# Kernel tuning notes

Hardware: AMD Instinct MI355X
Metric: run time of the kernel (lower is better)

Reference implementation:

```python
import jax, jax.numpy as jnp
import numpy as np
from jax import lax

WS = 8
NH = 16

def _conv1x1(t, w):
    # w: (Cout, Cin), t: (B,C,H,W)
    return jnp.einsum('oc,bchw->bohw', w, t)

def _bn(t, g, b, m, v, eps=1e-5):
    s = g * lax.rsqrt(v + eps)
    return (t - m[:, None, None]) * s[:, None, None] + b[:, None, None]

def _forward(x, qkv_w, l2_w, bn2_g, bn2_b, bn2_m, bn2_v, wq, wk, wv, rel_x, rel_y,
             l1_bias, rel_table, dw_w, bnp_g, bnp_b, bnp_m, bnp_v, pw_w):
    B, C, H, W = x.shape
    ws, nh = WS, NH
    d = C // nh
    scale = d ** -0.5

    # ---- local2: 1x1 conv + BN (inference) ----
    local = _bn(_conv1x1(x, l2_w), bn2_g, bn2_b, bn2_m, bn2_v)

    # ---- local1: SelfAttentionConv2d, k=3, pad=1, groups=1 ----
    xp = jnp.pad(x, ((0, 0), (0, 0), (1, 1), (1, 1)))  # zero pad
    vq = _conv1x1(xp, wq)
    vk = _conv1x1(xp, wk)
    vv = _conv1x1(xp, wv)
    win_q = vq[:, :, 1:H + 1, 1:W + 1]  # center crop -> (B,C,H,W)
    def patches3(t):
        p = jnp.stack([t[:, :, i:i + H, j:j + W] for i in range(3) for j in range(3)], axis=-1)
        return p.reshape(B, C, H, W, 3, 3)
    pk = patches3(vk)
    pv = patches3(vv)
    rs = C // 2
    qx = jnp.einsum('bxhw,xk->bhwk', win_q[:, :rs], rel_x)  # (B,H,W,3)
    qy = jnp.einsum('byhw,yk->bhwk', win_q[:, rs:], rel_y)
    logits = jnp.einsum('bchw,bchwkl->bhwkl', win_q, pk)
    logits = logits + qx[:, :, :, None, :] + qy[:, :, :, :, None]
    a = jax.nn.softmax(logits.reshape(B, H, W, 9), axis=-1).reshape(B, H, W, 3, 3)
    local = local + jnp.einsum('bhwkl,bchwkl->bchw', a, pv) + l1_bias[None, :, None, None]

    # ---- windowed MHSA (H, W divisible by ws so pad() is a no-op) ----
    qkv = _conv1x1(x, qkv_w)  # (B, 3C, H, W)
    hh, ww = H // ws, W // ws
    t = qkv.reshape(B, 3, nh, d, hh, ws, ww, ws)
    t = t.transpose(1, 0, 4, 6, 2, 5, 7, 3).reshape(3, B * hh * ww, nh, ws * ws, d)
    q, k, v = t[0], t[1], t[2]
    dots = jnp.einsum('wnid,wnjd->wnij', q, k) * scale
    # relative position bias
    coords = np.stack(np.meshgrid(np.arange(ws), np.arange(ws), indexing='ij')).reshape(2, -1)
    rel = (coords[:, :, None] - coords[:, None, :]).transpose(1, 2, 0) + (ws - 1)
    idx = rel[..., 0] * (2 * ws - 1) + rel[..., 1]  # (ws*ws, ws*ws)
    rpb = rel_table[idx.reshape(-1)].reshape(ws * ws, ws * ws, nh).transpose(2, 0, 1)
    dots = dots + rpb[None]
    attn = jnp.einsum('wnij,wnjd->wnid', jax.nn.softmax(dots, axis=-1), v)
    attn = attn.reshape(B, hh, ww, nh, ws, ws, d).transpose(0, 3, 6, 1, 4, 2, 5).reshape(B, C, H, W)

    # ---- pooling edge-correction branches ----
    pad_h = jnp.pad(attn, ((0, 0), (0, 0), (0, 1), (0, 0)), mode='reflect')
    pad_w = jnp.pad(attn, ((0, 0), (0, 0), (0, 0), (0, 1)), mode='reflect')
    p = ws // 2 - 1
    mph = lax.reduce_window(pad_h, -jnp.inf, lax.max, (1, 1, ws, 1), (1, 1, 1, 1),
                            [(0, 0), (0, 0), (p, p), (0, 0)])
    mpw = lax.reduce_window(pad_w, -jnp.inf, lax.max, (1, 1, 1, ws), (1, 1, 1, 1),
                            [(0, 0), (0, 0), (0, 0), (p, p)])
    aph = lax.reduce_window(pad_h, 0.0, lax.add, (1, 1, ws, 1), (1, 1, 1, 1),
                            [(0, 0), (0, 0), (p, p), (0, 0)]) / ws
    apw = lax.reduce_window(pad_w, 0.0, lax.add, (1, 1, 1, ws), (1, 1, 1, 1),
                            [(0, 0), (0, 0), (0, 0), (p, p)]) / ws
    out = mph + mpw + aph + apw + local

    # ---- proj: reflect pad_out + depthwise 8x8 conv (pad 3) + BN + 1x1 ----
    out = jnp.pad(out, ((0, 0), (0, 0), (0, 1), (0, 1)), mode='reflect')
    out = lax.conv_general_dilated(out, dw_w, (1, 1), [(3, 3), (3, 3)],
                                   dimension_numbers=('NCHW', 'OIHW', 'NCHW'),
                                   feature_group_count=C)
    out = _bn(out, bnp_g, bnp_b, bnp_m, bnp_v)
    out = _conv1x1(out, pw_w)
    return out[:, :, :H, :W]


def setup_inputs() -> dict:
    key = jax.random.key(0)
    ks = jax.random.split(key, 20)
    C = 256
    n = lambda k, shp, s=1.0: jax.random.normal(k, shp, dtype=jnp.float32) * s
    u = lambda k, shp: jax.random.uniform(k, shp, dtype=jnp.float32, minval=0.5, maxval=1.5)
    fan = 1.0 / 16.0  # 1/sqrt(256)
    return {
        'x': n(ks[0], (2, C, 96, 96)),
        'qkv_w': n(ks[1], (3 * C, C), fan),
        'l2_w': n(ks[2], (C, C), fan),
        'bn2_g': u(ks[3], (C,)), 'bn2_b': n(ks[4], (C,), 0.1),
        'bn2_m': n(ks[5], (C,), 0.1), 'bn2_v': u(ks[6], (C,)),
        'wq': n(ks[7], (C, C), fan), 'wk': n(ks[8], (C, C), fan), 'wv': n(ks[9], (C, C), fan),
        'rel_x': n(ks[10], (C // 2, 3), 0.1), 'rel_y': n(ks[11], (C // 2, 3), 0.1),
        'l1_bias': n(ks[12], (C,), 0.05),
        'rel_table': n(ks[13], (15 * 15, NH), 0.02),
        'dw_w': n(ks[14], (C, 1, 8, 8), 1.0 / 8.0),
        'bnp_g': u(ks[15], (C,)), 'bnp_b': n(ks[16], (C,), 0.1),
        'bnp_m': n(ks[17], (C,), 0.1), 'bnp_v': u(ks[18], (C,)),
        'pw_w': n(ks[19], (C, C), fan),
    }


def reference(x, qkv_w, l2_w, bn2_g, bn2_b, bn2_m, bn2_v, wq, wk, wv, rel_x, rel_y,
              l1_bias, rel_table, dw_w, bnp_g, bnp_b, bnp_m, bnp_v, pw_w):
    return _forward(x, qkv_w, l2_w, bn2_g, bn2_b, bn2_m, bn2_v, wq, wk, wv, rel_x, rel_y,
                    l1_bias, rel_table, dw_w, bnp_g, bnp_b, bnp_m, bnp_v, pw_w)
```

## Files before the change

kernel.cpp:

```cpp
#include <hip/hip_runtime.h>
#include <math.h>


namespace {

constexpr int NP = 96 * 96;
constexpr int C  = 256;

typedef __bf16 bf16x8 __attribute__((ext_vector_type(8)));
typedef __bf16 bf16x4 __attribute__((ext_vector_type(4)));
typedef float  f32x4  __attribute__((ext_vector_type(4)));
typedef float  f32x16 __attribute__((ext_vector_type(16)));

__device__ __forceinline__ unsigned short f2bf_rne(float f) {
  unsigned u = __float_as_uint(f);
  u += 0x7FFFu + ((u >> 16) & 1u);
  return (unsigned short)(u >> 16);
}
__device__ __forceinline__ __bf16 f2bf16(float f) {
  unsigned short s = f2bf_rne(f);
  return *(__bf16*)&s;
}
__device__ __forceinline__ float bf2f(unsigned short s) {
  unsigned u = (unsigned)s << 16;
  return __uint_as_float(u);
}
__device__ __forceinline__ float4 bf4_to_f4(const unsigned short* p) {
  bf16x4 v = *(const bf16x4*)p;
  float4 r;
  r.x = (float)v[0]; r.y = (float)v[1]; r.z = (float)v[2]; r.w = (float)v[3];
  return r;
}

__global__ __launch_bounds__(256) void prep(
    const float* __restrict__ x,
    const float* __restrict__ l2, const float* __restrict__ q,
    const float* __restrict__ k,  const float* __restrict__ v,
    const float* __restrict__ qkv, const float* __restrict__ pw,
    unsigned short* __restrict__ XT, unsigned short* __restrict__ W7)
{
  __shared__ float tile[64][65];
  const int bx = blockIdx.x;
  const int t = threadIdx.x;
  if (bx < 2048) {
    const int row = bx;
    const float* src; int r;
    if      (row <  256) { src = l2;  r = row; }
    else if (row <  512) { src = q;   r = row - 256; }
    else if (row <  768) { src = k;   r = row - 512; }
    else if (row < 1024) { src = v;   r = row - 768; }
    else if (row < 1792) { src = qkv; r = row - 1024; }
    else                 { src = pw;  r = row - 1792; }
    W7[row * 256 + t] = f2bf_rne(src[r * 256 + t]);
    return;
  }
  const int xb = bx - 2048;
  const int p0 = (xb % 144) * 64;
  const int c0 = ((xb / 144) % 4) * 64;
  const int b  = xb / 576;
  const float* xb_p = x + (long)b * C * NP;
#pragma unroll
  for (int i = 0; i < 4; ++i) {
    int s = i * 256 + t;
    int c = s >> 4, p4 = s & 15;
    float4 vv = *(const float4*)&xb_p[(long)(c0 + c) * NP + p0 + p4 * 4];
    tile[c][p4 * 4 + 0] = vv.x;
    tile[c][p4 * 4 + 1] = vv.y;
    tile[c][p4 * 4 + 2] = vv.z;
    tile[c][p4 * 4 + 3] = vv.w;
  }
  __syncthreads();
  unsigned short* XTb = XT + (long)b * NP * 256;
#pragma unroll
  for (int i = 0; i < 2; ++i) {
    int s = i * 256 + t;
    int p = s >> 3, c8 = s & 7;
    unsigned short u[8];
#pragma unroll
    for (int e = 0; e < 8; ++e) u[e] = f2bf_rne(tile[c8 * 8 + e][p]);
    *(uint4*)&XTb[(long)(p0 + p) * 256 + c0 + c8 * 8] = *(const uint4*)u;
  }
}

__global__ __launch_bounds__(256) void xpose(
    const float* __restrict__ x, unsigned short* __restrict__ XT)
{
  __shared__ float tile[64][65];
  const int t = threadIdx.x;
  const int p0 = blockIdx.x * 64, c0 = blockIdx.y * 64, b = blockIdx.z;
  const float* xb = x + (long)b * C * NP;
#pragma unroll
  for (int i = 0; i < 4; ++i) {
    int s = i * 256 + t;
    int c = s >> 4, p4 = s & 15;
    float4 v = *(const float4*)&xb[(long)(c0 + c) * NP + p0 + p4 * 4];
    tile[c][p4 * 4 + 0] = v.x;
    tile[c][p4 * 4 + 1] = v.y;
    tile[c][p4 * 4 + 2] = v.z;
    tile[c][p4 * 4 + 3] = v.w;
  }
  __syncthreads();
  unsigned short* XTb = XT + (long)b * NP * 256;
#pragma unroll
  for (int i = 0; i < 2; ++i) {
    int s = i * 256 + t;
    int p = s >> 3, c8 = s & 7;
    unsigned short u[8];
#pragma unroll
    for (int e = 0; e < 8; ++e) u[e] = f2bf_rne(tile[c8 * 8 + e][p]);
    *(uint4*)&XTb[(long)(p0 + p) * 256 + c0 + c8 * 8] = *(const uint4*)u;
  }
}

__device__ __forceinline__ void gemm_bt_body(
    unsigned short* smemS,
    const unsigned short* __restrict__ W, const unsigned short* __restrict__ XTb,
    unsigned short* __restrict__ Ob, int Mstride, int m0, int n0)
{
  unsigned short* As = smemS;
  unsigned short* Bs = smemS + 4096;

  const int t = threadIdx.x;
  const int lane = t & 63, wid = t >> 6;
  const int wm = wid >> 1, wn = wid & 1;
  const int l15 = lane & 15, l4 = lane >> 4;
  const int crow = lane >> 2;
  const int ccol = (lane & 3) * 8;

  f32x4 acc[4][4];
#pragma unroll
  for (int i = 0; i < 4; ++i)
#pragma unroll
    for (int j = 0; j < 4; ++j) acc[i][j] = (f32x4){0.f, 0.f, 0.f, 0.f};

  for (int k0 = 0; k0 < 256; k0 += 32) {
#pragma unroll
    for (int i = 0; i < 4; ++i) {
      const int ch = wid * 4 + i;
      if (ch < 8) {
        const int row = ch * 16 + crow;
        __builtin_amdgcn_global_load_lds(
            (const __attribute__((address_space(1))) unsigned int*)
                &W[(long)(m0 + row) * 256 + k0 + ccol],
            (__attribute__((address_space(3))) unsigned int*)&As[ch * 512],
            16, 0, 0);
      } else {
        const int row = (ch - 8) * 16 + crow;
        __builtin_amdgcn_global_load_lds(
            (const __attribute__((address_space(1))) unsigned int*)
                &XTb[(long)(n0 + row) * 256 + k0 + ccol],
            (__attribute__((address_space(3))) unsigned int*)&Bs[(ch - 8) * 512],
            16, 0, 0);
      }
    }
    __syncthreads();

    bf16x8 af[4], bb[4];
#pragma unroll
    for (int mf = 0; mf < 4; ++mf)
      af[mf] = *(const bf16x8*)&As[(wm * 64 + mf * 16 + l15) * 32 + l4 * 8];
#pragma unroll
    for (int nf = 0; nf < 4; ++nf)
      bb[nf] = *(const bf16x8*)&Bs[(wn * 64 + nf * 16 + l15) * 32 + l4 * 8];
#pragma unroll
    for (int mf = 0; mf < 4; ++mf)
#pragma unroll
      for (int nf = 0; nf < 4; ++nf)
        acc[mf][nf] = __builtin_amdgcn_mfma_f32_16x16x32_bf16(
            af[mf], bb[nf], acc[mf][nf], 0, 0, 0);
    __syncthreads();
  }

  unsigned short* trw = smemS + wid * 64 * 72;
#pragma unroll
  for (int mf = 0; mf < 4; ++mf)
#pragma unroll
    for (int nf = 0; nf < 4; ++nf) {
      unsigned u0 = (unsigned)f2bf_rne(acc[mf][nf][0]) |
                    ((unsigned)f2bf_rne(acc[mf][nf][1]) << 16);
      unsigned u1 = (unsigned)f2bf_rne(acc[mf][nf][2]) |
                    ((unsigned)f2bf_rne(acc[mf][nf][3]) << 16);
      uint2 uu; uu.x = u0; uu.y = u1;
      *(uint2*)&trw[(nf * 16 + l15) * 72 + mf * 16 + l4 * 4] = uu;
    }
  __syncthreads();

  const long pix = n0 + wn * 64 + lane;
  const long rowbase = pix * Mstride + m0 + wm * 64;
#pragma unroll
  for (int cc = 0; cc < 8; ++cc)
    *(uint4*)&Ob[rowbase + cc * 8] = *(const uint4*)&trw[lane * 72 + cc * 8];
}

__global__ __launch_bounds__(256) void gemm_bt(
    const unsigned short* __restrict__ W, const unsigned short* __restrict__ XT,
    unsigned short* __restrict__ O, int Mstride)
{
  __shared__ __align__(16) unsigned short smemS[18432];
  gemm_bt_body(smemS, W, XT + (long)blockIdx.z * NP * 256,
               O + (long)blockIdx.z * NP * Mstride, Mstride,
               blockIdx.y * 128, blockIdx.x * 128);
}

__device__ __forceinline__ void local_attn_body(
    char* smem,
    const unsigned short* __restrict__ GA, int b, int tile,
    const float* __restrict__ rel_x, const float* __restrict__ rel_y,
    const float* __restrict__ bn2_g, const float* __restrict__ bn2_b,
    const float* __restrict__ bn2_m, const float* __restrict__ bn2_v,
    const float* __restrict__ l1_bias, unsigned short* __restrict__ localO)
{
  float (*red)[32][13] = reinterpret_cast<float(*)[32][13]>(smem);
  float* srel  = (float*)(smem + 13312);
  float* sS    = (float*)(smem + 16384);
  float* sO    = sS + 256;
  float* sBias = sO + 256;

  const int t = threadIdx.x;
  const int px = t & 31, ch = t >> 5;
  const int ty = tile / 24, tx = tile % 24;
  const int h = ty * 8 + (px >> 2), w = tx * 4 + (px & 3);
  const int p = h * 96 + w;
  const unsigned short* Gb = GA + (long)b * NP * 1024;

  if (t < 128) {
    srel[t * 3 + 0] = rel_x[t * 3 + 0];
    srel[t * 3 + 1] = rel_x[t * 3 + 1];
    srel[t * 3 + 2] = rel_x[t * 3 + 2];
  } else {
    int r = t - 128;
    srel[t * 3 + 0] = rel_y[r * 3 + 0];
    srel[t * 3 + 1] = rel_y[r * 3 + 1];
    srel[t * 3 + 2] = rel_y[r * 3 + 2];
  }
  {
    float s = bn2_g[t] * rsqrtf(bn2_v[t] + 1e-5f);
    sS[t] = s;
    sO[t] = bn2_b[t] - bn2_m[t] * s;
    sBias[t] = l1_bias[t];
  }

  int nof[9];
  float msk[9];
#pragma unroll
  for (int ky = 0; ky < 3; ++ky)
#pragma unroll
    for (int kx = 0; kx < 3; ++kx) {
      int j = ky * 3 + kx, hn = h + ky - 1, wn = w + kx - 1;
      bool v = (hn >= 0 && hn < 96 && wn >= 0 && wn < 96);
      nof[j] = v ? hn * 96 + wn : p;
      msk[j] = v ? 1.f : 0.f;
    }
  __syncthreads();

  float lg[9] = {0, 0, 0, 0, 0, 0, 0, 0, 0};
  float rq[3] = {0, 0, 0};
  const int c0 = ch * 32;
#pragma unroll
  for (int i = 0; i < 4; ++i) {
    const int c = c0 + i * 8;
    bf16x8 q8 = *(const bf16x8*)&Gb[(long)p * 1024 + 256 + c];
    float qv[8];
#pragma unroll
    for (int e = 0; e < 8; ++e) qv[e] = (float)q8[e];
#pragma unroll
    for (int j = 0; j < 9; ++j) {
      bf16x8 k8 = *(const bf16x8*)&Gb[(long)nof[j] * 1024 + 512 + c];
#pragma unroll
      for (int e = 0; e < 8; ++e) lg[j] += qv[e] * (float)k8[e];
    }
#pragma unroll
    for (int e = 0; e < 8; ++e) {
      const float* sr = &srel[(c + e) * 3];
      rq[0] += qv[e] * sr[0];
      rq[1] += qv[e] * sr[1];
      rq[2] += qv[e] * sr[2];
    }
  }
#pragma unroll
  for (int j = 0; j < 9; ++j) red[ch][px][j] = lg[j] * msk[j];
#pragma unroll
  for (int l = 0; l < 3; ++l) red[ch][px][9 + l] = rq[l];
  __syncthreads();

  float a[9];
  float mx = -1e30f;
#pragma unroll
  for (int j = 0; j < 9; ++j) {
    float v = 0.f;
#pragma unroll
    for (int u = 0; u < 8; ++u) v += red[u][px][j];
    float qxl = red[0][px][9 + j % 3] + red[1][px][9 + j % 3] +
                red[2][px][9 + j % 3] + red[3][px][9 + j % 3];
    float qyk = red[4][px][9 + j / 3] + red[5][px][9 + j / 3] +
                red[6][px][9 + j / 3] + red[7][px][9 + j / 3];
    a[j] = v + qxl + qyk;
    mx = fmaxf(mx, a[j]);
  }
  float sum = 0.f;
#pragma unroll
  for (int j = 0; j < 9; ++j) { a[j] = __expf(a[j] - mx); sum += a[j]; }
  const float inv = 1.f / sum;
  float am[9];
#pragma unroll
  for (int j = 0; j < 9; ++j) am[j] = a[j] * inv * msk[j];

#pragma unroll
  for (int i = 0; i < 4; ++i) {
    const int c = c0 + i * 8;
    bf16x8 l28 = *(const bf16x8*)&Gb[(long)p * 1024 + 0 + c];
    float o8[8] = {0, 0, 0, 0, 0, 0, 0, 0};
#pragma unroll
    for (int j = 0; j < 9; ++j) {
      bf16x8 v8 = *(const bf16x8*)&Gb[(long)nof[j] * 1024 + 768 + c];
#pragma unroll
      for (int e = 0; e < 8; ++e) o8[e] += am[j] * (float)v8[e];
    }
#pragma unroll
    for (int e = 0; e < 8; ++e) {
      const int cg = c + e;
      localO[((long)b * C + cg) * NP + p] = f2bf_rne(
          (float)l28[e] * sS[cg] + sO[cg] + o8[e] + sBias[cg]);
    }
  }
}

__global__ __launch_bounds__(256) void la_qkv(
    const unsigned short* __restrict__ Wqkv, const unsigned short* __restrict__ XT,
    unsigned short* __restrict__ GB, const unsigned short* __restrict__ GA,
    const float* __restrict__ rel_x, const float* __restrict__ rel_y,
    const float* __restrict__ bn2_g, const float* __restrict__ bn2_b,
    const float* __restrict__ bn2_m, const float* __restrict__ bn2_v,
    const float* __restrict__ l1_bias, unsigned short* __restrict__ localO)
{
  __shared__ __align__(16) char smem[36864];
  const int bx = blockIdx.x;
  if (bx < 864) {
    const int n = bx % 72, rest = bx / 72;
    const int m = rest % 6, b = rest / 6;
    gemm_bt_body((unsigned short*)smem, Wqkv, XT + (long)b * NP * 256,
                 GB + (long)b * NP * 768, 768, m * 128, n * 128);
  } else {
    const int idx = bx - 864;
    const int orig = idx % 288, b = idx / 288;
    const int tile = (orig & 7) * 36 + (orig >> 3);
    local_attn_body(smem, GA, b, tile, rel_x, rel_y, bn2_g, bn2_b, bn2_m,
                    bn2_v, l1_bias, localO);
  }
}

__global__ __launch_bounds__(256) void gemm_cf32(
    const unsigned short* __restrict__ W, const unsigned short* __restrict__ XT,
    float* __restrict__ Co)
{
  __shared__ unsigned short As[64][40];
  __shared__ unsigned short Bs[128][40];

  const int t = threadIdx.x;
  const int lane = t & 63, wid = t >> 6;
  const int wm = wid >> 1, wn = wid & 1;
  const int l15 = lane & 15, l4 = lane >> 4;
  const int n0 = blockIdx.x * 128, m0 = blockIdx.y * 64;
  const unsigned short* XTb = XT + (long)blockIdx.z * NP * 256;
  float* Cb = Co + (long)blockIdx.z * C * NP;

  f32x4 acc[2][4];
#pragma unroll
  for (int i = 0; i < 2; ++i)
#pragma unroll
    for (int j = 0; j < 4; ++j) acc[i][j] = (f32x4){0.f, 0.f, 0.f, 0.f};

  for (int k0 = 0; k0 < 256; k0 += 32) {
    {
      int r = t >> 2, kc = t & 3;
      *(uint4*)&As[r][kc * 8] =
          *(const uint4*)&W[(long)(m0 + r) * 256 + k0 + kc * 8];
    }
#pragma unroll
    for (int i = 0; i < 2; ++i) {
      int s = i * 256 + t, r = s >> 2, kc = s & 3;
      *(uint4*)&Bs[r][kc * 8] =
          *(const uint4*)&XTb[(long)(n0 + r) * 256 + k0 + kc * 8];
    }
    __syncthreads();

    bf16x8 af[2], bb[4];
#pragma unroll
    for (int mf = 0; mf < 2; ++mf)
      af[mf] = *(const bf16x8*)&As[wm * 32 + mf * 16 + l15][l4 * 8];
#pragma unroll
    for (int nf = 0; nf < 4; ++nf)
      bb[nf] = *(const bf16x8*)&Bs[wn * 64 + nf * 16 + l15][l4 * 8];
#pragma unroll
    for (int mf = 0; mf < 2; ++mf)
#pragma unroll
      for (int nf = 0; nf < 4; ++nf)
        acc[mf][nf] = __builtin_amdgcn_mfma_f32_16x16x32_bf16(
            af[mf], bb[nf], acc[mf][nf], 0, 0, 0);
    __syncthreads();
  }

#pragma unroll
  for (int mf = 0; mf < 2; ++mf)
#pragma unroll
    for (int r = 0; r < 4; ++r) {
      int row = m0 + wm * 32 + mf * 16 + l4 * 4 + r;
#pragma unroll
      for (int nf = 0; nf < 4; ++nf) {
        int col = n0 + wn * 64 + nf * 16 + l15;
        Cb[(long)row * NP + col] = acc[mf][nf][r];
      }
    }
}

__global__ __launch_bounds__(64) void window_attn_mfma(
    const unsigned short* __restrict__ QKV,
    const float* __restrict__ rel_table, unsigned short* __restrict__ attnO)
{
  const int win = blockIdx.x, hd = blockIdx.y, b = blockIdx.z;
  const int wy = win / 12, wx = win % 12;
  const int lane = threadIdx.x;
  const int l15 = lane & 15, hi4 = lane >> 4;
  const int l31 = lane & 31, hi2 = lane >> 5;

  __shared__ float srpb[225];
  __shared__ __bf16 P[64][72];

  for (int i = lane; i < 225; i += 64) srpb[i] = rel_table[i * 16 + hd];

  const __bf16* base = (const __bf16*)QKV + (long)b * 9216 * 768;
  const int pixbase = (wy * 8) * 96 + wx * 8;

#define WPIX(i) (pixbase + ((i) >> 3) * 96 + ((i) & 7))

  bf16x8 kf[2], qf[2];
#pragma unroll
  for (int kt = 0; kt < 2; ++kt)
    kf[kt] = *(const bf16x8*)&base[(long)WPIX(32 * kt + l31) * 768 + 256 +
                                   hd * 16 + hi2 * 8];
#pragma unroll
  for (int qt = 0; qt < 2; ++qt)
    qf[qt] = *(const bf16x8*)&base[(long)WPIX(32 * qt + l31) * 768 +
                                   hd * 16 + hi2 * 8];

  bf16x8 vf[2];
#pragma unroll
  for (int kc = 0; kc < 2; ++kc)
#pragma unroll
    for (int j = 0; j < 8; ++j)
      vf[kc][j] = base[(long)WPIX(32 * kc + 8 * hi4 + j) * 768 + 512 +
                       hd * 16 + l15];

  f32x16 S[2][2];
#pragma unroll
  for (int kt = 0; kt < 2; ++kt)
#pragma unroll
    for (int qt = 0; qt < 2; ++qt)
#pragma unroll
      for (int r = 0; r < 16; ++r) S[kt][qt][r] = 0.f;

#pragma unroll
  for (int kt = 0; kt < 2; ++kt)
#pragma unroll
    for (int qt = 0; qt < 2; ++qt)
      S[kt][qt] = __builtin_amdgcn_mfma_f32_32x32x16_bf16(
          kf[kt], qf[qt], S[kt][qt], 0, 0, 0);

  __syncthreads();

  float mx[2] = {-1e30f, -1e30f};
#pragma unroll
  for (int kt = 0; kt < 2; ++kt)
#pragma unroll
    for (int r = 0; r < 16; ++r) {
      const int key = 32 * kt + (r & 3) + 8 * (r >> 2) + 4 * hi2;
      const int ky = key >> 3, kx = key & 7;
#pragma unroll
      for (int qt = 0; qt < 2; ++qt) {
        const int q = 32 * qt + l31;
        const int qy = q >> 3, qx = q & 7;
        float s = S[kt][qt][r] * 0.25f + srpb[(qy - ky + 7) * 15 + (qx - kx + 7)];
        S[kt][qt][r] = s;
        mx[qt] = fmaxf(mx[qt], s);
      }
    }
#pragma unroll
  for (int qt = 0; qt < 2; ++qt)
    mx[qt] = fmaxf(mx[qt], __shfl_xor(mx[qt], 32));

  float sum[2] = {0.f, 0.f};
#pragma unroll
  for (int kt = 0; kt < 2; ++kt)
#pragma unroll
    for (int qt = 0; qt < 2; ++qt)
#pragma unroll
      for (int r = 0; r < 16; ++r) {
        float e = __expf(S[kt][qt][r] - mx[qt]);
        S[kt][qt][r] = e;
        sum[qt] += e;
      }
#pragma unroll
  for (int qt = 0; qt < 2; ++qt) sum[qt] += __shfl_xor(sum[qt], 32);
  const float inv0 = 1.f / sum[0], inv1 = 1.f / sum[1];

#pragma unroll
  for (int qt = 0; qt < 2; ++qt) {
    const float inv = qt ? inv1 : inv0;
#pragma unroll
    for (int kt = 0; kt < 2; ++kt)
#pragma unroll
      for (int rq = 0; rq < 4; ++rq) {
        bf16x4 pk;
#pragma unroll
        for (int j = 0; j < 4; ++j) pk[j] = f2bf16(S[kt][qt][rq * 4 + j] * inv);
        *(bf16x4*)&P[32 * qt + l31][32 * kt + 8 * rq + 4 * hi2] = pk;
      }
  }
  __syncthreads();

  f32x4 o[4];
#pragma unroll
  for (int qt4 = 0; qt4 < 4; ++qt4) o[qt4] = (f32x4){0.f, 0.f, 0.f, 0.f};
#pragma unroll
  for (int kc = 0; kc < 2; ++kc)
#pragma unroll
    for (int qt4 = 0; qt4 < 4; ++qt4) {
      bf16x8 pf = *(const bf16x8*)&P[16 * qt4 + l15][32 * kc + 8 * hi4];
      o[qt4] = __builtin_amdgcn_mfma_f32_16x16x32_bf16(vf[kc], pf, o[qt4], 0, 0, 0);
    }

#pragma unroll
  for (int qt4 = 0; qt4 < 4; ++qt4)
#pragma unroll
    for (int r = 0; r < 4; ++r) {
      const int q = 16 * qt4 + l15;
      attnO[((long)b * C + hd * 16 + 4 * hi4 + r) * NP + WPIX(q)] =
          f2bf_rne(o[qt4][r]);
    }
#undef WPIX
}

__global__ __launch_bounds__(128) void pool_dw8(
    const unsigned short* __restrict__ attn,
    const unsigned short* __restrict__ localO,
    const float* __restrict__ dww,
    const float* __restrict__ bnp_g, const float* __restrict__ bnp_b,
    const float* __restrict__ bnp_m, const float* __restrict__ bnp_v,
    float* __restrict__ dst)
{
  const int r0 = blockIdx.x * 12;
  const int c = blockIdx.y, b = blockIdx.z;
  const int t = threadIdx.x;

  __shared__ float img[26 * 116];
  __shared__ float img2[19 * 108];

  const unsigned short* A = attn + ((long)b * C + c) * NP;
  const unsigned short* L = localO + ((long)b * C + c) * NP;

  for (int idx = t; idx < 26 * 28; idx += 128) {
    const int j = idx / 28, k = idx % 28;
    const int R = r0 - 6 + j;
    const bool rv = (R >= 0 && R <= 96);
    const int Rc = (R == 96) ? 94 : (rv ? R : 0);
    const int s0 = 4 * k - 8;
    float4 v = {-1e30f, -1e30f, -1e30f, -1e30f};
    if (rv && s0 >= 0 && s0 <= 92) v = bf4_to_f4(&A[Rc * 96 + s0]);
    else if (rv && s0 == 96) v.x = bf2f(A[Rc * 96 + 94]);
    *(float4*)&img[j * 116 + 4 * k] = v;
  }
  for (int idx = t; idx < 19 * 27; idx += 128) {
    const int j2 = idx / 27, g = idx % 27;
    const int R2 = r0 - 3 + j2;
    const bool rv = (R2 >= 0 && R2 <= 96);
    const int R2c = (R2 == 96) ? 94 : (rv ? R2 : 0);
    const int w0 = 4 * g - 4;
    float4 v = {0.f, 0.f, 0.f, 0.f};
    if (rv) {
      if (w0 >= 0 && w0 <= 92) v = bf4_to_f4(&L[R2c * 96 + w0]);
      else if (w0 == 96) v.x = bf2f(L[R2c * 96 + 94]);
    }
    *(float4*)&img2[j2 * 108 + 4 * g] = v;
  }
  float wr[64];
#pragma unroll
  for (int i = 0; i < 64; ++i) wr[i] = dww[c * 64 + i];
  const float scl = bnp_g[c] * rsqrtf(bnp_v[c] + 1e-5f);
  const float off = bnp_b[c] - bnp_m[c] * scl;
  __syncthreads();

  const int j2lo = (r0 == 0) ? 3 : 0;
  const int j2hi = (r0 == 84) ? 14 : 18;
  if (t < 120) {
    const int blk = t / 24, G = t % 24;
    const int j2b = j2lo + blk * 4;
    if (j2b <= j2hi) {
      float4 hc[11];
#pragma unroll
      for (int ii = 0; ii < 11; ++ii) {
        int rr = j2b + ii;
        rr = (rr > 25) ? 25 : rr;
        hc[ii] = *(const float4*)&img[rr * 116 + 4 * G + 8];
      }
#pragma unroll
      for (int r = 0; r < 4; ++r) {
        const int j2 = j2b + r;
        if (j2 > j2hi) break;
        float mph[4] = {-1e30f, -1e30f, -1e30f, -1e30f};
        float aph[4] = {0.f, 0.f, 0.f, 0.f};
#pragma unroll
        for (int ii = 0; ii < 8; ++ii) {
          const float h4[4] = {hc[r + ii].x, hc[r + ii].y, hc[r + ii].z,
                               hc[r + ii].w};
#pragma unroll
          for (int d = 0; d < 4; ++d) {
            mph[d] = fmaxf(mph[d], h4[d]);
            aph[d] += (h4[d] > -1e29f) ? h4[d] : 0.f;
          }
        }
        float rw[12];
        {
          const float* row = &img[(j2 + 3) * 116 + 4 * G + 4];
          float4 a0 = *(const float4*)&row[0];
          float4 a1 = *(const float4*)&row[4];
          float4 a2 = *(const float4*)&row[8];
          rw[0] = a0.x; rw[1] = a0.y; rw[2] = a0.z; rw[3] = a0.w;
          rw[4] = a1.x; rw[5] = a1.y; rw[6] = a1.z; rw[7] = a1.w;
          rw[8] = a2.x; rw[9] = a2.y; rw[10] = a2.z; rw[11] = a2.w;
        }
        float4 lv = *(const float4*)&img2[j2 * 108 + 4 * G + 4];
        const float l4[4] = {lv.x, lv.y, lv.z, lv.w};
        float o4[4];
#pragma unroll
        for (int d = 0; d < 4; ++d) {
          float mpw = -1e30f, apw = 0.f;
#pragma unroll
          for (int ii = 0; ii < 8; ++ii) {
            const float wv = rw[d + 1 + ii];
            mpw = fmaxf(mpw, wv);
            apw += (wv > -1e29f) ? wv : 0.f;
          }
          o4[d] = mph[d] + mpw + (aph[d] + apw) * 0.125f + l4[d];
        }
        float4 out;
        out.x = o4[0]; out.y = o4[1]; out.z = o4[2]; out.w = o4[3];
        *(float4*)&img2[j2 * 108 + 4 * G + 4] = out;
        if (G == 23) img2[j2 * 108 + 100] = o4[2];
        if (r0 == 84 && j2 == 13) {
          *(float4*)&img2[15 * 108 + 4 * G + 4] = out;
          if (G == 23) img2[15 * 108 + 100] = o4[2];
        }
      }
    }
  }
  __syncthreads();

  if (t < 72) {
    const int cb = t / 24, ocg = t % 24;
    const int hh0 = cb * 4;
    float acc[4][4];
#pragma unroll
    for (int o = 0; o < 4; ++o)
#pragma unroll
      for (int d = 0; d < 4; ++d) acc[o][d] = 0.f;
#pragma unroll
    for (int i = 0; i < 11; ++i) {
      const float* row = &img2[(hh0 + i) * 108 + 4 * ocg];
      float w12[12];
      {
        float4 a0 = *(const float4*)&row[0];
        float4 a1 = *(const float4*)&row[4];
        float4 a2 = *(const float4*)&row[8];
        w12[0] = a0.x; w12[1] = a0.y; w12[2] = a0.z; w12[3] = a0.w;
        w12[4] = a1.x; w12[5] = a1.y; w12[6] = a1.z; w12[7] = a1.w;
        w12[8] = a2.x; w12[9] = a2.y; w12[10] = a2.z; w12[11] = a2.w;
      }
#pragma unroll
      for (int o = 0; o < 4; ++o) {
        if (o > i || i - o > 7) continue;
        const int ir = i - o;
#pragma unroll
        for (int d = 0; d < 4; ++d)
#pragma unroll
          for (int jj = 0; jj < 8; ++jj)
            acc[o][d] = fmaf(wr[ir * 8 + jj], w12[d + 1 + jj], acc[o][d]);
      }
    }
#pragma unroll
    for (int o = 0; o < 4; ++o) {
      float4 s;
      s.x = acc[o][0] * scl + off;
      s.y = acc[o][1] * scl + off;
      s.z = acc[o][2] * scl + off;
      s.w = acc[o][3] * scl + off;
      *(float4*)&dst[((long)b * C + c) * NP + (r0 + hh0 + o) * 96 + 4 * ocg] = s;
    }
  }
}

}

extern "C" void kernel_launch(void* const* d_in, const int* in_sizes, int n_in,
                              void* d_out, int out_size, void* d_ws, size_t ws_size,
                              hipStream_t stream) {
  const float* x         = (const float*)d_in[0];
  const float* qkv_w     = (const float*)d_in[1];
  const float* l2_w      = (const float*)d_in[2];
  const float* bn2_g     = (const float*)d_in[3];
  const float* bn2_b     = (const float*)d_in[4];
  const float* bn2_m     = (const float*)d_in[5];
  const float* bn2_v     = (const float*)d_in[6];
  const float* wq        = (const float*)d_in[7];
  const float* wk        = (const float*)d_in[8];
  const float* wv        = (const float*)d_in[9];
  const float* rel_x     = (const float*)d_in[10];
  const float* rel_y     = (const float*)d_in[11];
  const float* l1_bias   = (const float*)d_in[12];
  const float* rel_table = (const float*)d_in[13];
  const float* dw_w      = (const float*)d_in[14];
  const float* bnp_g     = (const float*)d_in[15];
  const float* bnp_b     = (const float*)d_in[16];
  const float* bnp_m     = (const float*)d_in[17];
  const float* bnp_v     = (const float*)d_in[18];
  const float* pw_w      = (const float*)d_in[19];
  float* out = (float*)d_out;
  float* ws  = (float*)d_ws;

  unsigned short* GA     = (unsigned short*)ws;
  unsigned short* GB     = (unsigned short*)(ws + 9437184);
  unsigned short* localB = (unsigned short*)(ws + 16515072);
  unsigned short* W7     = (unsigned short*)(ws + 18874368);
  unsigned short* XT     = (unsigned short*)(ws + 19136512);
  unsigned short* attnB  = (unsigned short*)(ws + 19136512);
  float*          dwB    = ws;
  unsigned short* XT2    = (unsigned short*)(ws + 4718592);

  prep<<<dim3(3200), 256, 0, stream>>>(x, l2_w, wq, wk, wv, qkv_w, pw_w,
                                       XT, W7);

  gemm_bt<<<dim3(72, 8, 2), 256, 0, stream>>>(W7, XT, GA, 1024);

  la_qkv<<<dim3(1440), 256, 0, stream>>>(W7 + 1024 * 256, XT, GB, GA,
                                         rel_x, rel_y, bn2_g, bn2_b, bn2_m,
                                         bn2_v, l1_bias, localB);

  window_attn_mfma<<<dim3(144, 16, 2), 64, 0, stream>>>(GB, rel_table, attnB);

  pool_dw8<<<dim3(8, 256, 2), 128, 0, stream>>>(attnB, localB, dw_w, bnp_g,
                                                bnp_b, bnp_m, bnp_v, dwB);

  xpose<<<dim3(144, 4, 2), 256, 0, stream>>>(dwB, XT2);

  gemm_cf32<<<dim3(72, 4, 2), 256, 0, stream>>>(W7 + 1792 * 256, XT2, out);
}
```

Before: 166.9 us.

## Halve GEMM epilogue LDS staging and interleave GEMM/local-attention blocks

The GEMM epilogue now stages the bf16 transpose in two passes of 32 pixels per wave, so the shared buffer shrinks from 36 KB to about 18 KB. This allows more resident blocks per CU. The fused la_qkv kernel also interleaves its block indices in a 3:2 pattern of GEMM to local-attention blocks instead of running all GEMM blocks first. The goal is to mix compute-bound and memory-bound work on each CU. The two-pass epilogue uses narrower per-lane stores, and the pass loop has no explicit barrier, which relies on the wave writing and reading its own region.

```diff
diff --git a/kernel.cpp b/kernel.cpp
--- a/kernel.cpp
+++ b/kernel.cpp
@@ -171,32 +171,38 @@
     __syncthreads();
   }
 
-  unsigned short* trw = smemS + wid * 64 * 72;
-#pragma unroll
-  for (int mf = 0; mf < 4; ++mf)
-#pragma unroll
-    for (int nf = 0; nf < 4; ++nf) {
-      unsigned u0 = (unsigned)f2bf_rne(acc[mf][nf][0]) |
-                    ((unsigned)f2bf_rne(acc[mf][nf][1]) << 16);
-      unsigned u1 = (unsigned)f2bf_rne(acc[mf][nf][2]) |
-                    ((unsigned)f2bf_rne(acc[mf][nf][3]) << 16);
-      uint2 uu; uu.x = u0; uu.y = u1;
-      *(uint2*)&trw[(nf * 16 + l15) * 72 + mf * 16 + l4 * 4] = uu;
-    }
-  __syncthreads();
-
-  const long pix = n0 + wn * 64 + lane;
-  const long rowbase = pix * Mstride + m0 + wm * 64;
-#pragma unroll
-  for (int cc = 0; cc < 8; ++cc)
-    *(uint4*)&Ob[rowbase + cc * 8] = *(const uint4*)&trw[lane * 72 + cc * 8];
+  unsigned short* trw = smemS + wid * 2304;
+  const int lp = lane >> 1;
+  const int cbase = (lane & 1) * 4;
+#pragma unroll
+  for (int pass = 0; pass < 2; ++pass) {
+#pragma unroll
+    for (int nfh = 0; nfh < 2; ++nfh) {
+      const int nf = pass * 2 + nfh;
+#pragma unroll
+      for (int mf = 0; mf < 4; ++mf) {
+        unsigned u0 = (unsigned)f2bf_rne(acc[mf][nf][0]) |
+                      ((unsigned)f2bf_rne(acc[mf][nf][1]) << 16);
+        unsigned u1 = (unsigned)f2bf_rne(acc[mf][nf][2]) |
+                      ((unsigned)f2bf_rne(acc[mf][nf][3]) << 16);
+        uint2 uu; uu.x = u0; uu.y = u1;
+        *(uint2*)&trw[(nfh * 16 + l15) * 72 + mf * 16 + l4 * 4] = uu;
+      }
+    }
+    const long pix = n0 + wn * 64 + pass * 32 + lp;
+    const long rowbase = pix * Mstride + m0 + wm * 64;
+#pragma unroll
+    for (int cc = 0; cc < 4; ++cc)
+      *(uint4*)&Ob[rowbase + (cbase + cc) * 8] =
+          *(const uint4*)&trw[lp * 72 + (cbase + cc) * 8];
+  }
 }
 
 __global__ __launch_bounds__(256) void gemm_bt(
     const unsigned short* __restrict__ W, const unsigned short* __restrict__ XT,
     unsigned short* __restrict__ O, int Mstride)
 {
-  __shared__ __align__(16) unsigned short smemS[18432];
+  __shared__ __align__(16) unsigned short smemS[9216];
   gemm_bt_body(smemS, W, XT + (long)blockIdx.z * NP * 256,
                O + (long)blockIdx.z * NP * Mstride, Mstride,
                blockIdx.y * 128, blockIdx.x * 128);
@@ -333,16 +339,18 @@
     const float* __restrict__ bn2_m, const float* __restrict__ bn2_v,
     const float* __restrict__ l1_bias, unsigned short* __restrict__ localO)
 {
-  __shared__ __align__(16) char smem[36864];
+  __shared__ __align__(16) char smem[19456];
   const int bx = blockIdx.x;
-  if (bx < 864) {
-    const int n = bx % 72, rest = bx / 72;
+  const int g = bx / 5, r = bx % 5;
+  if (r < 3) {
+    const int gi = g * 3 + r;
+    const int n = gi % 72, rest = gi / 72;
     const int m = rest % 6, b = rest / 6;
     gemm_bt_body((unsigned short*)smem, Wqkv, XT + (long)b * NP * 256,
                  GB + (long)b * NP * 768, 768, m * 128, n * 128);
   } else {
-    const int idx = bx - 864;
-    const int orig = idx % 288, b = idx / 288;
+    const int li = g * 2 + (r - 3);
+    const int orig = li % 288, b = li / 288;
     const int tile = (orig & 7) * 36 + (orig >> 3);
     local_attn_body(smem, GA, b, tile, rel_x, rel_y, bn2_g, bn2_b, bn2_m,
                     bn2_v, l1_bias, localO);
```

After: 162.7 us, median of 2. -2.5%, faster.
